# Performance work log

Hardware: AMD Instinct MI355X
Metric: run time of the kernel (lower is better)

## Reference

```python
import jax, jax.numpy as jnp
import numpy as np
import math

D_MODEL, HEADS, KQ = 1024, 16, 64
B, S = 2, 2048

def setup_inputs() -> dict:
    key = jax.random.key(0)
    k1, k2, k3, k4, k5 = jax.random.split(key, 5)
    scale = D_MODEL ** (-0.5)
    return {
        "x_BSE": jax.random.normal(k1, (B, S, D_MODEL), dtype=jnp.float32),
        "w_q": jax.random.normal(k2, (D_MODEL, HEADS, KQ), dtype=jnp.float32) * scale,
        "w_k": jax.random.normal(k3, (D_MODEL, HEADS, KQ), dtype=jnp.float32) * scale,
        "w_v": jax.random.normal(k4, (D_MODEL, HEADS, KQ), dtype=jnp.float32) * scale,
        "w_o": jax.random.normal(k5, (D_MODEL, HEADS, KQ), dtype=jnp.float32) * scale,
    }

def reference(x_BSE, w_q, w_k, w_v, w_o):
    # QKV projections (self-attention: memory = x)
    q_BSHK = jnp.einsum('BSE,EHK->BSHK', x_BSE, w_q)
    k_BMHK = jnp.einsum('BSE,EHK->BSHK', x_BSE, w_k)
    v_BMHK = jnp.einsum('BSE,EHK->BSHK', x_BSE, w_v)
    logits_BSHM = jnp.einsum('BSHK,BMHK->BSHM', q_BSHK, k_BMHK) / math.sqrt(KQ)
    # causal (diagonal) mask: query position >= memory position
    Sdim, Mdim = logits_BSHM.shape[1], logits_BSHM.shape[3]
    qpos = jnp.arange(Sdim)[:, None]          # [S,1]
    mpos = jnp.arange(Mdim)[None, :]          # [1,M]
    mask_SM = jnp.where(qpos >= mpos, 0.0, -jnp.inf).astype(logits_BSHM.dtype)
    logits_BSHM = logits_BSHM + mask_SM[None, :, None, :]
    probs_BSHM = jax.nn.softmax(logits_BSHM, axis=3)
    out_BSHK = jnp.einsum('BSHM,BMHK->BSHK', probs_BSHM, v_BMHK)
    return jnp.einsum('BSHK,EHK->BSE', out_BSHK, w_o)
```

## Files before the change

### kernel.cpp

```cpp
#include <hip/hip_runtime.h>
#include <hip/hip_bf16.h>

typedef __attribute__((ext_vector_type(4)))  float f32x4;
typedef __attribute__((ext_vector_type(16))) float f32x16;
typedef __attribute__((ext_vector_type(8)))  short short8;
typedef __attribute__((ext_vector_type(4)))  short short4v;

__device__ __forceinline__ short f2bf(float f) {
  union { float f; unsigned u; } x; x.f = f;
  unsigned r = (x.u + 0x7FFFu + ((x.u >> 16) & 1u)) >> 16;
  return (short)r;
}
__device__ __forceinline__ unsigned cvtpk(float lo, float hi) {
  unsigned r;
  asm("v_cvt_pk_bf16_f32 %0, %1, %2" : "=v"(r) : "v"(lo), "v"(hi));
  return r;
}

__global__ __launch_bounds__(256) void k_cast(const float* __restrict__ in,
                                              short* __restrict__ out, int n4) {
  int i = blockIdx.x * 256 + threadIdx.x;
  if (i >= n4) return;
  f32x4 v = ((const f32x4*)in)[i];
  short4v s;
  s[0] = f2bf(v[0]); s[1] = f2bf(v[1]); s[2] = f2bf(v[2]); s[3] = f2bf(v[3]);
  ((short4v*)out)[i] = s;
}

__global__ __launch_bounds__(256) void k_pack(const float* __restrict__ wq,
                                              const float* __restrict__ wk,
                                              const float* __restrict__ wv,
                                              short* __restrict__ WT) {
  int nt = blockIdx.x, et = blockIdx.y, sel = blockIdx.z;
  const float* w = sel == 0 ? wq : (sel == 1 ? wk : wv);
  __shared__ float tile[64][65];
  int tid = threadIdx.x;
  int cl = tid & 63, rw = tid >> 6;
#pragma unroll
  for (int j = 0; j < 16; ++j) {
    int el = j * 4 + rw;
    tile[el][cl] = w[(size_t)(et * 64 + el) * 1024 + nt * 64 + cl];
  }
  __syncthreads();
#pragma unroll
  for (int j = 0; j < 16; ++j) {
    int nl = j * 4 + rw;
    int n = sel * 1024 + nt * 64 + nl;
    WT[(size_t)n * 1024 + et * 64 + cl] = f2bf(tile[cl][nl]);
  }
}

template <int EPI>
__global__ __launch_bounds__(256) void k_gemm(const short* __restrict__ A,
                                              const short* __restrict__ B,
                                              short* __restrict__ Qo, short* __restrict__ Ko,
                                              short* __restrict__ Vo, float* __restrict__ out,
                                              int M, int N, int K) {
  __shared__ short As[128][40];
  __shared__ short Bs[128][40];
  int tid = threadIdx.x;
  int bm = blockIdx.y * 128, bn = blockIdx.x * 128;
  int wid = tid >> 6, lane = tid & 63;
  int wm = (wid >> 1) * 64, wn = (wid & 1) * 64;
  int lg = lane >> 4, lr = lane & 15;
  f32x4 acc[4][4] = {};

  int sr = tid >> 2, sc = tid & 3;
  const short* Ar0 = A + (size_t)(bm + sr) * K;
  const short* Ar1 = A + (size_t)(bm + sr + 64) * K;
  const short* Br0 = B + (size_t)(bn + sr) * K;
  const short* Br1 = B + (size_t)(bn + sr + 64) * K;

  short8 pa0 = *(const short8*)&Ar0[sc * 8];
  short8 pa1 = *(const short8*)&Ar1[sc * 8];
  short8 pb0 = *(const short8*)&Br0[sc * 8];
  short8 pb1 = *(const short8*)&Br1[sc * 8];

  int nk = K >> 5;
  for (int kt = 0; kt < nk; ++kt) {
    __syncthreads();
    *(short8*)&As[sr][sc * 8] = pa0;
    *(short8*)&As[sr + 64][sc * 8] = pa1;
    *(short8*)&Bs[sr][sc * 8] = pb0;
    *(short8*)&Bs[sr + 64][sc * 8] = pb1;
    if (kt + 1 < nk) {
      int ko = (kt + 1) * 32;
      pa0 = *(const short8*)&Ar0[ko + sc * 8];
      pa1 = *(const short8*)&Ar1[ko + sc * 8];
      pb0 = *(const short8*)&Br0[ko + sc * 8];
      pb1 = *(const short8*)&Br1[ko + sc * 8];
    }
    __syncthreads();
    short8 af[4], bf_[4];
#pragma unroll
    for (int mt = 0; mt < 4; ++mt)
      af[mt] = *(const short8*)&As[wm + mt * 16 + lr][lg * 8];
#pragma unroll
    for (int ntl = 0; ntl < 4; ++ntl)
      bf_[ntl] = *(const short8*)&Bs[wn + ntl * 16 + lr][lg * 8];
#pragma unroll
    for (int mt = 0; mt < 4; ++mt)
#pragma unroll
      for (int ntl = 0; ntl < 4; ++ntl)
        acc[mt][ntl] = __builtin_amdgcn_mfma_f32_16x16x32_bf16(af[mt], bf_[ntl], acc[mt][ntl], 0, 0, 0);
  }

#pragma unroll
  for (int mt = 0; mt < 4; ++mt)
#pragma unroll
    for (int ntl = 0; ntl < 4; ++ntl)
#pragma unroll
      for (int rr = 0; rr < 4; ++rr) {
        int m = bm + wm + mt * 16 + lg * 4 + rr;
        int n = bn + wn + ntl * 16 + lr;
        float val = acc[mt][ntl][rr];
        if (EPI == 0) {
          int b = m >> 11, s = m & 2047;
          int sel = n >> 10, hk = n & 1023;
          int h = hk >> 6, kd = hk & 63;
          if (sel == 0) Qo[((size_t)(b * 16 + h) * 2048 + s) * 64 + kd] = f2bf(val * 0.18033688011112042f);
          else if (sel == 1) Ko[((size_t)(b * 16 + h) * 2048 + s) * 64 + kd] = f2bf(val);
          else Vo[((size_t)(b * 16 + h) * 64 + kd) * 2048 + s] = f2bf(val);
        } else {
          out[(size_t)m * 1024 + n] = val;
        }
      }
}

__global__ __launch_bounds__(128, 2) void k_attn(const short* __restrict__ Q,
                                                 const short* __restrict__ K,
                                                 const short* __restrict__ VT,
                                                 short* __restrict__ O) {
  const int S = 2048;
  int bh = blockIdx.x;
  int g = 31 - blockIdx.y;

  int tid = threadIdx.x;
  int wid = tid >> 6, lane = tid & 63;
  int hi = lane >> 5, ln = lane & 31;
  int qw = 2 * g + wid;
  int ntile = qw + 1;
  int tmax = 2 * g + 2;
  int q_g = qw * 32 + ln;

  __shared__ short Ks[2][32][64];
  __shared__ short Vs[2][64][32];

  const short* Qb = Q + (size_t)bh * S * 64;
  const short* Kb = K + (size_t)bh * S * 64;
  const short* Vb = VT + (size_t)bh * 64 * S;

  short8 qf[4];
#pragma unroll
  for (int ds = 0; ds < 4; ++ds)
    qf[ds] = *(const short8*)&Qb[(size_t)q_g * 64 + ds * 16 + hi * 8];

  int kr = tid >> 2, kcb = tid & 3;
  int vd = tid >> 1, vcb = tid & 1;
  const short* kgp = Kb + (size_t)kr * 64;
  const short* vgp = Vb + (size_t)vd * S;

  short8 kreg0 = *(const short8*)&kgp[(size_t)0 + kcb * 8];
  short8 kreg1 = *(const short8*)&kgp[(size_t)0 + (kcb + 4) * 8];
  short8 vreg0 = *(const short8*)&vgp[(size_t)0 + vcb * 8];
  short8 vreg1 = *(const short8*)&vgp[(size_t)0 + (vcb + 2) * 8];

  f32x16 acoA = {}, acoB = {};
  float l = 0.f;

  for (int t = 0; t < tmax; ++t) {
    int buf = t & 1;
    *(short8*)&Ks[buf][kr][(kcb ^ (kr & 7)) * 8]       = kreg0;
    *(short8*)&Ks[buf][kr][((kcb + 4) ^ (kr & 7)) * 8] = kreg1;
    *(short8*)&Vs[buf][vd][(vcb ^ (vd & 3)) * 8]       = vreg0;
    *(short8*)&Vs[buf][vd][((vcb + 2) ^ (vd & 3)) * 8] = vreg1;
    if (t + 1 < tmax) {
      size_t ko = (size_t)(t + 1) * 32 * 64;
      size_t vo = (size_t)(t + 1) * 32;
      kreg0 = *(const short8*)&kgp[ko + kcb * 8];
      kreg1 = *(const short8*)&kgp[ko + (kcb + 4) * 8];
      vreg0 = *(const short8*)&vgp[vo + vcb * 8];
      vreg1 = *(const short8*)&vgp[vo + (vcb + 2) * 8];
    }
    __syncthreads();

    if (t < ntile) {
      short8 kc0 = *(const short8*)&Ks[buf][ln][((0 + hi) ^ (ln & 7)) * 8];
      short8 kc1 = *(const short8*)&Ks[buf][ln][((2 + hi) ^ (ln & 7)) * 8];
      short8 kc2 = *(const short8*)&Ks[buf][ln][((4 + hi) ^ (ln & 7)) * 8];
      short8 kc3 = *(const short8*)&Ks[buf][ln][((6 + hi) ^ (ln & 7)) * 8];
      f32x16 sa = {};
      __builtin_amdgcn_s_setprio(1);
      sa = __builtin_amdgcn_mfma_f32_32x32x16_bf16(kc0, qf[0], sa, 0, 0, 0);
      sa = __builtin_amdgcn_mfma_f32_32x32x16_bf16(kc1, qf[1], sa, 0, 0, 0);
      sa = __builtin_amdgcn_mfma_f32_32x32x16_bf16(kc2, qf[2], sa, 0, 0, 0);
      sa = __builtin_amdgcn_mfma_f32_32x32x16_bf16(kc3, qf[3], sa, 0, 0, 0);
      __builtin_amdgcn_s_setprio(0);

      if (t == qw) {
#pragma unroll
        for (int r = 0; r < 16; ++r) {
          int kv_g = t * 32 + (r & 3) + 8 * (r >> 2) + 4 * hi;
          if (kv_g > q_g) sa[r] = -1e30f;
        }
      }

      short8 v00 = *(const short8*)&Vs[buf][ln][((0 + hi) ^ (ln & 3)) * 8];
      short8 v01 = *(const short8*)&Vs[buf][ln][((2 + hi) ^ (ln & 3)) * 8];
      short8 v10 = *(const short8*)&Vs[buf][32 + ln][((0 + hi) ^ (ln & 3)) * 8];
      short8 v11 = *(const short8*)&Vs[buf][32 + ln][((2 + hi) ^ (ln & 3)) * 8];

      float p[16];
#pragma unroll
      for (int r = 0; r < 16; ++r) p[r] = exp2f(sa[r]);
      float s0 = (p[0] + p[1]) + (p[2] + p[3]);
      float s1 = (p[4] + p[5]) + (p[6] + p[7]);
      float s2 = (p[8] + p[9]) + (p[10] + p[11]);
      float s3 = (p[12] + p[13]) + (p[14] + p[15]);
      l += (s0 + s1) + (s2 + s3);

#pragma unroll
      for (int s = 0; s < 2; ++s) {
        unsigned c0 = cvtpk(p[8 * s + 0], p[8 * s + 1]);
        unsigned c1 = cvtpk(p[8 * s + 2], p[8 * s + 3]);
        unsigned c2 = cvtpk(p[8 * s + 4], p[8 * s + 5]);
        unsigned c3 = cvtpk(p[8 * s + 6], p[8 * s + 7]);
        unsigned pc0 = (unsigned)__shfl_xor((int)c0, 32);
        unsigned pc1 = (unsigned)__shfl_xor((int)c1, 32);
        unsigned pc2 = (unsigned)__shfl_xor((int)c2, 32);
        unsigned pc3 = (unsigned)__shfl_xor((int)c3, 32);
        union { unsigned u[4]; short8 v; } pb;
        pb.u[0] = hi ? pc2 : c0;
        pb.u[1] = hi ? pc3 : c1;
        pb.u[2] = hi ? c2 : pc0;
        pb.u[3] = hi ? c3 : pc1;
        __builtin_amdgcn_s_setprio(1);
        if (s == 0) {
          acoA = __builtin_amdgcn_mfma_f32_32x32x16_bf16(v00, pb.v, acoA, 0, 0, 0);
          acoB = __builtin_amdgcn_mfma_f32_32x32x16_bf16(v10, pb.v, acoB, 0, 0, 0);
        } else {
          acoA = __builtin_amdgcn_mfma_f32_32x32x16_bf16(v01, pb.v, acoA, 0, 0, 0);
          acoB = __builtin_amdgcn_mfma_f32_32x32x16_bf16(v11, pb.v, acoB, 0, 0, 0);
        }
        __builtin_amdgcn_s_setprio(0);
      }
    }
  }

  l += __shfl_xor(l, 32);
  float rl = 1.f / l;
  int b = bh >> 4, h = bh & 15;
  size_t obase = ((size_t)b * 2048 + q_g) * 1024 + h * 64;
#pragma unroll
  for (int g4 = 0; g4 < 4; ++g4) {
    int d0 = 8 * g4 + 4 * hi;
    *(unsigned*)&O[obase + d0]          = cvtpk(acoA[4 * g4] * rl, acoA[4 * g4 + 1] * rl);
    *(unsigned*)&O[obase + d0 + 2]      = cvtpk(acoA[4 * g4 + 2] * rl, acoA[4 * g4 + 3] * rl);
    *(unsigned*)&O[obase + 32 + d0]     = cvtpk(acoB[4 * g4] * rl, acoB[4 * g4 + 1] * rl);
    *(unsigned*)&O[obase + 32 + d0 + 2] = cvtpk(acoB[4 * g4 + 2] * rl, acoB[4 * g4 + 3] * rl);
  }
}

extern "C" void kernel_launch(void* const* d_in, const int* in_sizes, int n_in,
                              void* d_out, int out_size, void* d_ws, size_t ws_size,
                              hipStream_t stream) {
  const float* x  = (const float*)d_in[0];
  const float* wq = (const float*)d_in[1];
  const float* wk = (const float*)d_in[2];
  const float* wv = (const float*)d_in[3];
  const float* wo = (const float*)d_in[4];
  float* out = (float*)d_out;
  char* ws = (char*)d_ws;

  short* x_bf  = (short*)(ws);
  short* WqkvT = (short*)(ws + ((size_t)8 << 20));
  short* wo_bf = (short*)(ws + ((size_t)14 << 20));
  short* Qb    = (short*)(ws + ((size_t)16 << 20));
  short* Kb    = (short*)(ws + ((size_t)24 << 20));
  short* Vt    = (short*)(ws + ((size_t)32 << 20));
  short* Ob    = (short*)(ws + ((size_t)40 << 20));

  k_cast<<<4096, 256, 0, stream>>>(x, x_bf, 1048576);
  k_cast<<<1024, 256, 0, stream>>>(wo, wo_bf, 262144);
  k_pack<<<dim3(16, 16, 3), 256, 0, stream>>>(wq, wk, wv, WqkvT);
  k_gemm<0><<<dim3(24, 32), 256, 0, stream>>>(x_bf, WqkvT, Qb, Kb, Vt, nullptr, 4096, 3072, 1024);
  k_attn<<<dim3(32, 32), 128, 0, stream>>>(Qb, Kb, Vt, Ob);
  k_gemm<1><<<dim3(8, 32), 256, 0, stream>>>(Ob, wo_bf, nullptr, nullptr, nullptr, out, 4096, 1024, 1024);
}
```

Measured before the change: 130.9 us.

## Split causal attention KV range in two halves and merge partials

```diff
diff --git a/kernel.cpp b/kernel.cpp
--- a/kernel.cpp
+++ b/kernel.cpp
@@ -10,6 +10,10 @@
   union { float f; unsigned u; } x; x.f = f;
   unsigned r = (x.u + 0x7FFFu + ((x.u >> 16) & 1u)) >> 16;
   return (short)r;
+}
+__device__ __forceinline__ float bf2f(short s) {
+  union { unsigned u; float f; } x; x.u = ((unsigned)(unsigned short)s) << 16;
+  return x.f;
 }
 __device__ __forceinline__ unsigned cvtpk(float lo, float hi) {
   unsigned r;
@@ -127,21 +131,26 @@
       }
 }
 
-__global__ __launch_bounds__(128, 2) void k_attn(const short* __restrict__ Q,
+__global__ __launch_bounds__(128, 4) void k_attn(const short* __restrict__ Q,
                                                  const short* __restrict__ K,
                                                  const short* __restrict__ VT,
-                                                 short* __restrict__ O) {
+                                                 short* __restrict__ P0,
+                                                 short* __restrict__ P1,
+                                                 float* __restrict__ ML) {
   const int S = 2048;
   int bh = blockIdx.x;
-  int g = 31 - blockIdx.y;
+  int y = blockIdx.y;
+  int h = y & 1;
+  int g = 31 - (y >> 1);
 
   int tid = threadIdx.x;
   int wid = tid >> 6, lane = tid & 63;
   int hi = lane >> 5, ln = lane & 31;
   int qw = 2 * g + wid;
-  int ntile = qw + 1;
-  int tmax = 2 * g + 2;
   int q_g = qw * 32 + ln;
+  int tb = h * (g + 1);
+  int nstage = g + 1;
+  int te_w = qw + 1;
 
   __shared__ short Ks[2][32][64];
   __shared__ short Vs[2][64][32];
@@ -160,22 +169,25 @@
   const short* kgp = Kb + (size_t)kr * 64;
   const short* vgp = Vb + (size_t)vd * S;
 
-  short8 kreg0 = *(const short8*)&kgp[(size_t)0 + kcb * 8];
-  short8 kreg1 = *(const short8*)&kgp[(size_t)0 + (kcb + 4) * 8];
-  short8 vreg0 = *(const short8*)&vgp[(size_t)0 + vcb * 8];
-  short8 vreg1 = *(const short8*)&vgp[(size_t)0 + (vcb + 2) * 8];
+  size_t ko0 = (size_t)tb * 2048;
+  size_t vo0 = (size_t)tb * 32;
+  short8 kreg0 = *(const short8*)&kgp[ko0 + kcb * 8];
+  short8 kreg1 = *(const short8*)&kgp[ko0 + (kcb + 4) * 8];
+  short8 vreg0 = *(const short8*)&vgp[vo0 + vcb * 8];
+  short8 vreg1 = *(const short8*)&vgp[vo0 + (vcb + 2) * 8];
 
   f32x16 acoA = {}, acoB = {};
   float l = 0.f;
 
-  for (int t = 0; t < tmax; ++t) {
-    int buf = t & 1;
+  for (int i = 0; i < nstage; ++i) {
+    int t = tb + i;
+    int buf = i & 1;
     *(short8*)&Ks[buf][kr][(kcb ^ (kr & 7)) * 8]       = kreg0;
     *(short8*)&Ks[buf][kr][((kcb + 4) ^ (kr & 7)) * 8] = kreg1;
     *(short8*)&Vs[buf][vd][(vcb ^ (vd & 3)) * 8]       = vreg0;
     *(short8*)&Vs[buf][vd][((vcb + 2) ^ (vd & 3)) * 8] = vreg1;
-    if (t + 1 < tmax) {
-      size_t ko = (size_t)(t + 1) * 32 * 64;
+    if (i + 1 < nstage) {
+      size_t ko = (size_t)(t + 1) * 2048;
       size_t vo = (size_t)(t + 1) * 32;
       kreg0 = *(const short8*)&kgp[ko + kcb * 8];
       kreg1 = *(const short8*)&kgp[ko + (kcb + 4) * 8];
@@ -184,7 +196,7 @@
     }
     __syncthreads();
 
-    if (t < ntile) {
+    if (t < te_w) {
       short8 kc0 = *(const short8*)&Ks[buf][ln][((0 + hi) ^ (ln & 7)) * 8];
       short8 kc1 = *(const short8*)&Ks[buf][ln][((2 + hi) ^ (ln & 7)) * 8];
       short8 kc2 = *(const short8*)&Ks[buf][ln][((4 + hi) ^ (ln & 7)) * 8];
@@ -248,17 +260,44 @@
   }
 
   l += __shfl_xor(l, 32);
-  float rl = 1.f / l;
-  int b = bh >> 4, h = bh & 15;
-  size_t obase = ((size_t)b * 2048 + q_g) * 1024 + h * 64;
+  int row = (bh << 11) + q_g;
+  ML[row * 2 + h] = l;
+  short* Op = h ? P1 : P0;
+  size_t base = (size_t)row * 64;
 #pragma unroll
   for (int g4 = 0; g4 < 4; ++g4) {
     int d0 = 8 * g4 + 4 * hi;
-    *(unsigned*)&O[obase + d0]          = cvtpk(acoA[4 * g4] * rl, acoA[4 * g4 + 1] * rl);
-    *(unsigned*)&O[obase + d0 + 2]      = cvtpk(acoA[4 * g4 + 2] * rl, acoA[4 * g4 + 3] * rl);
-    *(unsigned*)&O[obase + 32 + d0]     = cvtpk(acoB[4 * g4] * rl, acoB[4 * g4 + 1] * rl);
-    *(unsigned*)&O[obase + 32 + d0 + 2] = cvtpk(acoB[4 * g4 + 2] * rl, acoB[4 * g4 + 3] * rl);
-  }
+    *(unsigned*)&Op[base + d0]          = cvtpk(acoA[4 * g4], acoA[4 * g4 + 1]);
+    *(unsigned*)&Op[base + d0 + 2]      = cvtpk(acoA[4 * g4 + 2], acoA[4 * g4 + 3]);
+    *(unsigned*)&Op[base + 32 + d0]     = cvtpk(acoB[4 * g4], acoB[4 * g4 + 1]);
+    *(unsigned*)&Op[base + 32 + d0 + 2] = cvtpk(acoB[4 * g4 + 2], acoB[4 * g4 + 3]);
+  }
+}
+
+__global__ __launch_bounds__(256) void k_merge(const short* __restrict__ P0,
+                                               const short* __restrict__ P1,
+                                               const float* __restrict__ ML,
+                                               short* __restrict__ O) {
+  int gi = blockIdx.x * 256 + threadIdx.x;
+  int row = gi >> 2;
+  int dc = (gi & 3) << 4;
+  float w = 1.f / (ML[row * 2] + ML[row * 2 + 1]);
+  size_t pbase = (size_t)row * 64 + dc;
+  short8 a0 = *(const short8*)&P0[pbase];
+  short8 a1 = *(const short8*)&P0[pbase + 8];
+  short8 b0 = *(const short8*)&P1[pbase];
+  short8 b1 = *(const short8*)&P1[pbase + 8];
+  int bh = row >> 11, q = row & 2047;
+  int b = bh >> 4, h = bh & 15;
+  size_t obase = ((size_t)b * 2048 + q) * 1024 + h * 64 + dc;
+  short8 o0, o1;
+#pragma unroll
+  for (int j = 0; j < 8; ++j) {
+    o0[j] = f2bf((bf2f(a0[j]) + bf2f(b0[j])) * w);
+    o1[j] = f2bf((bf2f(a1[j]) + bf2f(b1[j])) * w);
+  }
+  *(short8*)&O[obase] = o0;
+  *(short8*)&O[obase + 8] = o1;
 }
 
 extern "C" void kernel_launch(void* const* d_in, const int* in_sizes, int n_in,
@@ -279,11 +318,15 @@
   short* Kb    = (short*)(ws + ((size_t)24 << 20));
   short* Vt    = (short*)(ws + ((size_t)32 << 20));
   short* Ob    = (short*)(ws + ((size_t)40 << 20));
+  short* P0    = (short*)(ws);
+  float* ML    = (float*)(ws + ((size_t)8 << 20));
+  short* P1    = (short*)(ws + ((size_t)48 << 20));
 
   k_cast<<<4096, 256, 0, stream>>>(x, x_bf, 1048576);
   k_cast<<<1024, 256, 0, stream>>>(wo, wo_bf, 262144);
   k_pack<<<dim3(16, 16, 3), 256, 0, stream>>>(wq, wk, wv, WqkvT);
   k_gemm<0><<<dim3(24, 32), 256, 0, stream>>>(x_bf, WqkvT, Qb, Kb, Vt, nullptr, 4096, 3072, 1024);
-  k_attn<<<dim3(32, 32), 128, 0, stream>>>(Qb, Kb, Vt, Ob);
+  k_attn<<<dim3(32, 64), 128, 0, stream>>>(Qb, Kb, Vt, P0, P1, ML);
+  k_merge<<<1024, 256, 0, stream>>>(P0, P1, ML, Ob);
   k_gemm<1><<<dim3(8, 32), 256, 0, stream>>>(Ob, wo_bf, nullptr, nullptr, nullptr, out, 4096, 1024, 1024);
 }
```

Result: slower. 138.5 us (+5.8%).

## Process KV tiles in pairs per barrier with interleaved QK MFMA chains

Applied to the files above, without the earlier changes.

```diff
diff --git a/kernel.cpp b/kernel.cpp
--- a/kernel.cpp
+++ b/kernel.cpp
@@ -139,12 +139,11 @@
   int wid = tid >> 6, lane = tid & 63;
   int hi = lane >> 5, ln = lane & 31;
   int qw = 2 * g + wid;
-  int ntile = qw + 1;
-  int tmax = 2 * g + 2;
   int q_g = qw * 32 + ln;
-
-  __shared__ short Ks[2][32][64];
-  __shared__ short Vs[2][64][32];
+  int npair = g + 1;
+
+  __shared__ short Ks[2][2][32][64];
+  __shared__ short Vs[2][2][64][32];
 
   const short* Qb = Q + (size_t)bh * S * 64;
   const short* Kb = K + (size_t)bh * S * 64;
@@ -160,87 +159,155 @@
   const short* kgp = Kb + (size_t)kr * 64;
   const short* vgp = Vb + (size_t)vd * S;
 
-  short8 kreg0 = *(const short8*)&kgp[(size_t)0 + kcb * 8];
-  short8 kreg1 = *(const short8*)&kgp[(size_t)0 + (kcb + 4) * 8];
-  short8 vreg0 = *(const short8*)&vgp[(size_t)0 + vcb * 8];
-  short8 vreg1 = *(const short8*)&vgp[(size_t)0 + (vcb + 2) * 8];
+  short8 ka0 = *(const short8*)&kgp[kcb * 8];
+  short8 ka1 = *(const short8*)&kgp[(kcb + 4) * 8];
+  short8 kb0 = *(const short8*)&kgp[2048 + kcb * 8];
+  short8 kb1 = *(const short8*)&kgp[2048 + (kcb + 4) * 8];
+  short8 va0 = *(const short8*)&vgp[vcb * 8];
+  short8 va1 = *(const short8*)&vgp[(vcb + 2) * 8];
+  short8 vb0 = *(const short8*)&vgp[32 + vcb * 8];
+  short8 vb1 = *(const short8*)&vgp[32 + (vcb + 2) * 8];
 
   f32x16 acoA = {}, acoB = {};
   float l = 0.f;
 
-  for (int t = 0; t < tmax; ++t) {
-    int buf = t & 1;
-    *(short8*)&Ks[buf][kr][(kcb ^ (kr & 7)) * 8]       = kreg0;
-    *(short8*)&Ks[buf][kr][((kcb + 4) ^ (kr & 7)) * 8] = kreg1;
-    *(short8*)&Vs[buf][vd][(vcb ^ (vd & 3)) * 8]       = vreg0;
-    *(short8*)&Vs[buf][vd][((vcb + 2) ^ (vd & 3)) * 8] = vreg1;
-    if (t + 1 < tmax) {
-      size_t ko = (size_t)(t + 1) * 32 * 64;
-      size_t vo = (size_t)(t + 1) * 32;
-      kreg0 = *(const short8*)&kgp[ko + kcb * 8];
-      kreg1 = *(const short8*)&kgp[ko + (kcb + 4) * 8];
-      vreg0 = *(const short8*)&vgp[vo + vcb * 8];
-      vreg1 = *(const short8*)&vgp[vo + (vcb + 2) * 8];
+  for (int p = 0; p < npair; ++p) {
+    int pb = p & 1;
+    *(short8*)&Ks[pb][0][kr][(kcb ^ (kr & 7)) * 8]       = ka0;
+    *(short8*)&Ks[pb][0][kr][((kcb + 4) ^ (kr & 7)) * 8] = ka1;
+    *(short8*)&Ks[pb][1][kr][(kcb ^ (kr & 7)) * 8]       = kb0;
+    *(short8*)&Ks[pb][1][kr][((kcb + 4) ^ (kr & 7)) * 8] = kb1;
+    *(short8*)&Vs[pb][0][vd][(vcb ^ (vd & 3)) * 8]       = va0;
+    *(short8*)&Vs[pb][0][vd][((vcb + 2) ^ (vd & 3)) * 8] = va1;
+    *(short8*)&Vs[pb][1][vd][(vcb ^ (vd & 3)) * 8]       = vb0;
+    *(short8*)&Vs[pb][1][vd][((vcb + 2) ^ (vd & 3)) * 8] = vb1;
+    if (p + 1 < npair) {
+      size_t ko0 = (size_t)(2 * p + 2) * 2048, ko1 = (size_t)(2 * p + 3) * 2048;
+      size_t vo0 = (size_t)(2 * p + 2) * 32,   vo1 = (size_t)(2 * p + 3) * 32;
+      ka0 = *(const short8*)&kgp[ko0 + kcb * 8];
+      ka1 = *(const short8*)&kgp[ko0 + (kcb + 4) * 8];
+      kb0 = *(const short8*)&kgp[ko1 + kcb * 8];
+      kb1 = *(const short8*)&kgp[ko1 + (kcb + 4) * 8];
+      va0 = *(const short8*)&vgp[vo0 + vcb * 8];
+      va1 = *(const short8*)&vgp[vo0 + (vcb + 2) * 8];
+      vb0 = *(const short8*)&vgp[vo1 + vcb * 8];
+      vb1 = *(const short8*)&vgp[vo1 + (vcb + 2) * 8];
     }
     __syncthreads();
 
-    if (t < ntile) {
-      short8 kc0 = *(const short8*)&Ks[buf][ln][((0 + hi) ^ (ln & 7)) * 8];
-      short8 kc1 = *(const short8*)&Ks[buf][ln][((2 + hi) ^ (ln & 7)) * 8];
-      short8 kc2 = *(const short8*)&Ks[buf][ln][((4 + hi) ^ (ln & 7)) * 8];
-      short8 kc3 = *(const short8*)&Ks[buf][ln][((6 + hi) ^ (ln & 7)) * 8];
-      f32x16 sa = {};
-      __builtin_amdgcn_s_setprio(1);
-      sa = __builtin_amdgcn_mfma_f32_32x32x16_bf16(kc0, qf[0], sa, 0, 0, 0);
-      sa = __builtin_amdgcn_mfma_f32_32x32x16_bf16(kc1, qf[1], sa, 0, 0, 0);
-      sa = __builtin_amdgcn_mfma_f32_32x32x16_bf16(kc2, qf[2], sa, 0, 0, 0);
-      sa = __builtin_amdgcn_mfma_f32_32x32x16_bf16(kc3, qf[3], sa, 0, 0, 0);
-      __builtin_amdgcn_s_setprio(0);
-
-      if (t == qw) {
-#pragma unroll
-        for (int r = 0; r < 16; ++r) {
-          int kv_g = t * 32 + (r & 3) + 8 * (r >> 2) + 4 * hi;
-          if (kv_g > q_g) sa[r] = -1e30f;
-        }
-      }
-
-      short8 v00 = *(const short8*)&Vs[buf][ln][((0 + hi) ^ (ln & 3)) * 8];
-      short8 v01 = *(const short8*)&Vs[buf][ln][((2 + hi) ^ (ln & 3)) * 8];
-      short8 v10 = *(const short8*)&Vs[buf][32 + ln][((0 + hi) ^ (ln & 3)) * 8];
-      short8 v11 = *(const short8*)&Vs[buf][32 + ln][((2 + hi) ^ (ln & 3)) * 8];
-
-      float p[16];
-#pragma unroll
-      for (int r = 0; r < 16; ++r) p[r] = exp2f(sa[r]);
-      float s0 = (p[0] + p[1]) + (p[2] + p[3]);
-      float s1 = (p[4] + p[5]) + (p[6] + p[7]);
-      float s2 = (p[8] + p[9]) + (p[10] + p[11]);
-      float s3 = (p[12] + p[13]) + (p[14] + p[15]);
-      l += (s0 + s1) + (s2 + s3);
-
+    int t0 = 2 * p, t1 = 2 * p + 1;
+
+    short8 kc00 = *(const short8*)&Ks[pb][0][ln][((0 + hi) ^ (ln & 7)) * 8];
+    short8 kc01 = *(const short8*)&Ks[pb][0][ln][((2 + hi) ^ (ln & 7)) * 8];
+    short8 kc02 = *(const short8*)&Ks[pb][0][ln][((4 + hi) ^ (ln & 7)) * 8];
+    short8 kc03 = *(const short8*)&Ks[pb][0][ln][((6 + hi) ^ (ln & 7)) * 8];
+    short8 kc10 = *(const short8*)&Ks[pb][1][ln][((0 + hi) ^ (ln & 7)) * 8];
+    short8 kc11 = *(const short8*)&Ks[pb][1][ln][((2 + hi) ^ (ln & 7)) * 8];
+    short8 kc12 = *(const short8*)&Ks[pb][1][ln][((4 + hi) ^ (ln & 7)) * 8];
+    short8 kc13 = *(const short8*)&Ks[pb][1][ln][((6 + hi) ^ (ln & 7)) * 8];
+
+    f32x16 sa0 = {}, sa1 = {};
+    __builtin_amdgcn_s_setprio(1);
+    sa0 = __builtin_amdgcn_mfma_f32_32x32x16_bf16(kc00, qf[0], sa0, 0, 0, 0);
+    sa1 = __builtin_amdgcn_mfma_f32_32x32x16_bf16(kc10, qf[0], sa1, 0, 0, 0);
+    sa0 = __builtin_amdgcn_mfma_f32_32x32x16_bf16(kc01, qf[1], sa0, 0, 0, 0);
+    sa1 = __builtin_amdgcn_mfma_f32_32x32x16_bf16(kc11, qf[1], sa1, 0, 0, 0);
+    sa0 = __builtin_amdgcn_mfma_f32_32x32x16_bf16(kc02, qf[2], sa0, 0, 0, 0);
+    sa1 = __builtin_amdgcn_mfma_f32_32x32x16_bf16(kc12, qf[2], sa1, 0, 0, 0);
+    sa0 = __builtin_amdgcn_mfma_f32_32x32x16_bf16(kc03, qf[3], sa0, 0, 0, 0);
+    sa1 = __builtin_amdgcn_mfma_f32_32x32x16_bf16(kc13, qf[3], sa1, 0, 0, 0);
+    __builtin_amdgcn_s_setprio(0);
+
+    if (t0 >= qw) {
+#pragma unroll
+      for (int r = 0; r < 16; ++r) {
+        int kv_g = t0 * 32 + (r & 3) + 8 * (r >> 2) + 4 * hi;
+        if (kv_g > q_g) sa0[r] = -1e30f;
+      }
+    }
+    if (t1 >= qw) {
+#pragma unroll
+      for (int r = 0; r < 16; ++r) {
+        int kv_g = t1 * 32 + (r & 3) + 8 * (r >> 2) + 4 * hi;
+        if (kv_g > q_g) sa1[r] = -1e30f;
+      }
+    }
+
+    float p0[16], p1[16];
+#pragma unroll
+    for (int r = 0; r < 16; ++r) p0[r] = exp2f(sa0[r]);
+#pragma unroll
+    for (int r = 0; r < 16; ++r) p1[r] = exp2f(sa1[r]);
+    {
+      float s00 = (p0[0] + p0[1]) + (p0[2] + p0[3]);
+      float s01 = (p0[4] + p0[5]) + (p0[6] + p0[7]);
+      float s02 = (p0[8] + p0[9]) + (p0[10] + p0[11]);
+      float s03 = (p0[12] + p0[13]) + (p0[14] + p0[15]);
+      float s10 = (p1[0] + p1[1]) + (p1[2] + p1[3]);
+      float s11 = (p1[4] + p1[5]) + (p1[6] + p1[7]);
+      float s12 = (p1[8] + p1[9]) + (p1[10] + p1[11]);
+      float s13 = (p1[12] + p1[13]) + (p1[14] + p1[15]);
+      l += ((s00 + s01) + (s02 + s03)) + ((s10 + s11) + (s12 + s13));
+    }
+
+    {
+      short8 v00 = *(const short8*)&Vs[pb][0][ln][((0 + hi) ^ (ln & 3)) * 8];
+      short8 v01 = *(const short8*)&Vs[pb][0][ln][((2 + hi) ^ (ln & 3)) * 8];
+      short8 v10 = *(const short8*)&Vs[pb][0][32 + ln][((0 + hi) ^ (ln & 3)) * 8];
+      short8 v11 = *(const short8*)&Vs[pb][0][32 + ln][((2 + hi) ^ (ln & 3)) * 8];
 #pragma unroll
       for (int s = 0; s < 2; ++s) {
-        unsigned c0 = cvtpk(p[8 * s + 0], p[8 * s + 1]);
-        unsigned c1 = cvtpk(p[8 * s + 2], p[8 * s + 3]);
-        unsigned c2 = cvtpk(p[8 * s + 4], p[8 * s + 5]);
-        unsigned c3 = cvtpk(p[8 * s + 6], p[8 * s + 7]);
+        unsigned c0 = cvtpk(p0[8 * s + 0], p0[8 * s + 1]);
+        unsigned c1 = cvtpk(p0[8 * s + 2], p0[8 * s + 3]);
+        unsigned c2 = cvtpk(p0[8 * s + 4], p0[8 * s + 5]);
+        unsigned c3 = cvtpk(p0[8 * s + 6], p0[8 * s + 7]);
         unsigned pc0 = (unsigned)__shfl_xor((int)c0, 32);
         unsigned pc1 = (unsigned)__shfl_xor((int)c1, 32);
         unsigned pc2 = (unsigned)__shfl_xor((int)c2, 32);
         unsigned pc3 = (unsigned)__shfl_xor((int)c3, 32);
-        union { unsigned u[4]; short8 v; } pb;
-        pb.u[0] = hi ? pc2 : c0;
-        pb.u[1] = hi ? pc3 : c1;
-        pb.u[2] = hi ? c2 : pc0;
-        pb.u[3] = hi ? c3 : pc1;
+        union { unsigned u[4]; short8 v; } pbv;
+        pbv.u[0] = hi ? pc2 : c0;
+        pbv.u[1] = hi ? pc3 : c1;
+        pbv.u[2] = hi ? c2 : pc0;
+        pbv.u[3] = hi ? c3 : pc1;
         __builtin_amdgcn_s_setprio(1);
         if (s == 0) {
-          acoA = __builtin_amdgcn_mfma_f32_32x32x16_bf16(v00, pb.v, acoA, 0, 0, 0);
-          acoB = __builtin_amdgcn_mfma_f32_32x32x16_bf16(v10, pb.v, acoB, 0, 0, 0);
+          acoA = __builtin_amdgcn_mfma_f32_32x32x16_bf16(v00, pbv.v, acoA, 0, 0, 0);
+          acoB = __builtin_amdgcn_mfma_f32_32x32x16_bf16(v10, pbv.v, acoB, 0, 0, 0);
         } else {
-          acoA = __builtin_amdgcn_mfma_f32_32x32x16_bf16(v01, pb.v, acoA, 0, 0, 0);
-          acoB = __builtin_amdgcn_mfma_f32_32x32x16_bf16(v11, pb.v, acoB, 0, 0, 0);
+          acoA = __builtin_amdgcn_mfma_f32_32x32x16_bf16(v01, pbv.v, acoA, 0, 0, 0);
+          acoB = __builtin_amdgcn_mfma_f32_32x32x16_bf16(v11, pbv.v, acoB, 0, 0, 0);
+        }
+        __builtin_amdgcn_s_setprio(0);
+      }
+    }
+    {
+      short8 v00 = *(const short8*)&Vs[pb][1][ln][((0 + hi) ^ (ln & 3)) * 8];
+      short8 v01 = *(const short8*)&Vs[pb][1][ln][((2 + hi) ^ (ln & 3)) * 8];
+      short8 v10 = *(const short8*)&Vs[pb][1][32 + ln][((0 + hi) ^ (ln & 3)) * 8];
+      short8 v11 = *(const short8*)&Vs[pb][1][32 + ln][((2 + hi) ^ (ln & 3)) * 8];
+#pragma unroll
+      for (int s = 0; s < 2; ++s) {
+        unsigned c0 = cvtpk(p1[8 * s + 0], p1[8 * s + 1]);
+        unsigned c1 = cvtpk(p1[8 * s + 2], p1[8 * s + 3]);
+        unsigned c2 = cvtpk(p1[8 * s + 4], p1[8 * s + 5]);
+        unsigned c3 = cvtpk(p1[8 * s + 6], p1[8 * s + 7]);
+        unsigned pc0 = (unsigned)__shfl_xor((int)c0, 32);
+        unsigned pc1 = (unsigned)__shfl_xor((int)c1, 32);
+        unsigned pc2 = (unsigned)__shfl_xor((int)c2, 32);
+        unsigned pc3 = (unsigned)__shfl_xor((int)c3, 32);
+        union { unsigned u[4]; short8 v; } pbv;
+        pbv.u[0] = hi ? pc2 : c0;
+        pbv.u[1] = hi ? pc3 : c1;
+        pbv.u[2] = hi ? c2 : pc0;
+        pbv.u[3] = hi ? c3 : pc1;
+        __builtin_amdgcn_s_setprio(1);
+        if (s == 0) {
+          acoA = __builtin_amdgcn_mfma_f32_32x32x16_bf16(v00, pbv.v, acoA, 0, 0, 0);
+          acoB = __builtin_amdgcn_mfma_f32_32x32x16_bf16(v10, pbv.v, acoB, 0, 0, 0);
+        } else {
+          acoA = __builtin_amdgcn_mfma_f32_32x32x16_bf16(v01, pbv.v, acoA, 0, 0, 0);
+          acoB = __builtin_amdgcn_mfma_f32_32x32x16_bf16(v11, pbv.v, acoB, 0, 0, 0);
         }
         __builtin_amdgcn_s_setprio(0);
       }
```

Measured after the change: 129.7 us. Within noise of the previous version (-0.9%).

## Process KV tiles in pairs with two-deep register prefetch in attention

Applied to the files above, without the earlier changes.

```diff
diff --git a/kernel.cpp b/kernel.cpp
--- a/kernel.cpp
+++ b/kernel.cpp
@@ -108,23 +108,34 @@
 #pragma unroll
   for (int mt = 0; mt < 4; ++mt)
 #pragma unroll
-    for (int ntl = 0; ntl < 4; ++ntl)
-#pragma unroll
-      for (int rr = 0; rr < 4; ++rr) {
-        int m = bm + wm + mt * 16 + lg * 4 + rr;
-        int n = bn + wn + ntl * 16 + lr;
-        float val = acc[mt][ntl][rr];
-        if (EPI == 0) {
-          int b = m >> 11, s = m & 2047;
-          int sel = n >> 10, hk = n & 1023;
-          int h = hk >> 6, kd = hk & 63;
-          if (sel == 0) Qo[((size_t)(b * 16 + h) * 2048 + s) * 64 + kd] = f2bf(val * 0.18033688011112042f);
-          else if (sel == 1) Ko[((size_t)(b * 16 + h) * 2048 + s) * 64 + kd] = f2bf(val);
-          else Vo[((size_t)(b * 16 + h) * 64 + kd) * 2048 + s] = f2bf(val);
+    for (int ntl = 0; ntl < 4; ++ntl) {
+      int m0 = bm + wm + mt * 16 + lg * 4;
+      int n = bn + wn + ntl * 16 + lr;
+      if (EPI == 0) {
+        int b = m0 >> 11, s0 = m0 & 2047;
+        int sel = n >> 10, hk = n & 1023;
+        int h = hk >> 6, kd = hk & 63;
+        if (sel == 0) {
+#pragma unroll
+          for (int rr = 0; rr < 4; ++rr)
+            Qo[((size_t)(b * 16 + h) * 2048 + s0 + rr) * 64 + kd] =
+                f2bf(acc[mt][ntl][rr] * 0.18033688011112042f);
+        } else if (sel == 1) {
+#pragma unroll
+          for (int rr = 0; rr < 4; ++rr)
+            Ko[((size_t)(b * 16 + h) * 2048 + s0 + rr) * 64 + kd] = f2bf(acc[mt][ntl][rr]);
         } else {
-          out[(size_t)m * 1024 + n] = val;
+          short4v v4;
+#pragma unroll
+          for (int rr = 0; rr < 4; ++rr) v4[rr] = f2bf(acc[mt][ntl][rr]);
+          *(short4v*)&Vo[((size_t)(b * 16 + h) * 64 + kd) * 2048 + s0] = v4;
         }
+      } else {
+#pragma unroll
+        for (int rr = 0; rr < 4; ++rr)
+          out[(size_t)(m0 + rr) * 1024 + n] = acc[mt][ntl][rr];
       }
+    }
 }
 
 __global__ __launch_bounds__(128, 2) void k_attn(const short* __restrict__ Q,
@@ -139,12 +150,11 @@
   int wid = tid >> 6, lane = tid & 63;
   int hi = lane >> 5, ln = lane & 31;
   int qw = 2 * g + wid;
-  int ntile = qw + 1;
-  int tmax = 2 * g + 2;
   int q_g = qw * 32 + ln;
-
-  __shared__ short Ks[2][32][64];
-  __shared__ short Vs[2][64][32];
+  int npair = g + 1;
+
+  __shared__ short Ks[2][2][32][64];
+  __shared__ short Vs[2][2][64][32];
 
   const short* Qb = Q + (size_t)bh * S * 64;
   const short* Kb = K + (size_t)bh * S * 64;
@@ -160,92 +170,172 @@
   const short* kgp = Kb + (size_t)kr * 64;
   const short* vgp = Vb + (size_t)vd * S;
 
-  short8 kreg0 = *(const short8*)&kgp[(size_t)0 + kcb * 8];
-  short8 kreg1 = *(const short8*)&kgp[(size_t)0 + (kcb + 4) * 8];
-  short8 vreg0 = *(const short8*)&vgp[(size_t)0 + vcb * 8];
-  short8 vreg1 = *(const short8*)&vgp[(size_t)0 + (vcb + 2) * 8];
+  short8 Aka0, Aka1, Akb0, Akb1, Ava0, Ava1, Avb0, Avb1;
+  short8 Bka0, Bka1, Bkb0, Bkb1, Bva0, Bva1, Bvb0, Bvb1;
+
+#define LOADP(SET, pn)                                                        \
+  {                                                                           \
+    size_t ko0 = (size_t)(2 * (pn)) * 2048, ko1 = (size_t)(2 * (pn) + 1) * 2048; \
+    size_t vo0 = (size_t)(2 * (pn)) * 32,   vo1 = (size_t)(2 * (pn) + 1) * 32;   \
+    SET##ka0 = *(const short8*)&kgp[ko0 + kcb * 8];                           \
+    SET##ka1 = *(const short8*)&kgp[ko0 + (kcb + 4) * 8];                     \
+    SET##kb0 = *(const short8*)&kgp[ko1 + kcb * 8];                           \
+    SET##kb1 = *(const short8*)&kgp[ko1 + (kcb + 4) * 8];                     \
+    SET##va0 = *(const short8*)&vgp[vo0 + vcb * 8];                           \
+    SET##va1 = *(const short8*)&vgp[vo0 + (vcb + 2) * 8];                     \
+    SET##vb0 = *(const short8*)&vgp[vo1 + vcb * 8];                           \
+    SET##vb1 = *(const short8*)&vgp[vo1 + (vcb + 2) * 8];                     \
+  }
+
+#define WRITEP(SET, BUF)                                                      \
+  {                                                                           \
+    *(short8*)&Ks[BUF][0][kr][(kcb ^ (kr & 7)) * 8]       = SET##ka0;         \
+    *(short8*)&Ks[BUF][0][kr][((kcb + 4) ^ (kr & 7)) * 8] = SET##ka1;         \
+    *(short8*)&Ks[BUF][1][kr][(kcb ^ (kr & 7)) * 8]       = SET##kb0;         \
+    *(short8*)&Ks[BUF][1][kr][((kcb + 4) ^ (kr & 7)) * 8] = SET##kb1;         \
+    *(short8*)&Vs[BUF][0][vd][(vcb ^ (vd & 3)) * 8]       = SET##va0;         \
+    *(short8*)&Vs[BUF][0][vd][((vcb + 2) ^ (vd & 3)) * 8] = SET##va1;         \
+    *(short8*)&Vs[BUF][1][vd][(vcb ^ (vd & 3)) * 8]       = SET##vb0;         \
+    *(short8*)&Vs[BUF][1][vd][((vcb + 2) ^ (vd & 3)) * 8] = SET##vb1;         \
+  }
 
   f32x16 acoA = {}, acoB = {};
   float l = 0.f;
 
-  for (int t = 0; t < tmax; ++t) {
-    int buf = t & 1;
-    *(short8*)&Ks[buf][kr][(kcb ^ (kr & 7)) * 8]       = kreg0;
-    *(short8*)&Ks[buf][kr][((kcb + 4) ^ (kr & 7)) * 8] = kreg1;
-    *(short8*)&Vs[buf][vd][(vcb ^ (vd & 3)) * 8]       = vreg0;
-    *(short8*)&Vs[buf][vd][((vcb + 2) ^ (vd & 3)) * 8] = vreg1;
-    if (t + 1 < tmax) {
-      size_t ko = (size_t)(t + 1) * 32 * 64;
-      size_t vo = (size_t)(t + 1) * 32;
-      kreg0 = *(const short8*)&kgp[ko + kcb * 8];
-      kreg1 = *(const short8*)&kgp[ko + (kcb + 4) * 8];
-      vreg0 = *(const short8*)&vgp[vo + vcb * 8];
-      vreg1 = *(const short8*)&vgp[vo + (vcb + 2) * 8];
+#define COMPUTE_PAIR(BUF, P)                                                  \
+  {                                                                           \
+    int t0 = 2 * (P), t1 = 2 * (P) + 1;                                       \
+    short8 kc00 = *(const short8*)&Ks[BUF][0][ln][((0 + hi) ^ (ln & 7)) * 8]; \
+    short8 kc01 = *(const short8*)&Ks[BUF][0][ln][((2 + hi) ^ (ln & 7)) * 8]; \
+    short8 kc02 = *(const short8*)&Ks[BUF][0][ln][((4 + hi) ^ (ln & 7)) * 8]; \
+    short8 kc03 = *(const short8*)&Ks[BUF][0][ln][((6 + hi) ^ (ln & 7)) * 8]; \
+    short8 kc10 = *(const short8*)&Ks[BUF][1][ln][((0 + hi) ^ (ln & 7)) * 8]; \
+    short8 kc11 = *(const short8*)&Ks[BUF][1][ln][((2 + hi) ^ (ln & 7)) * 8]; \
+    short8 kc12 = *(const short8*)&Ks[BUF][1][ln][((4 + hi) ^ (ln & 7)) * 8]; \
+    short8 kc13 = *(const short8*)&Ks[BUF][1][ln][((6 + hi) ^ (ln & 7)) * 8]; \
+    f32x16 sa0 = {}, sa1 = {};                                                \
+    __builtin_amdgcn_s_setprio(1);                                            \
+    sa0 = __builtin_amdgcn_mfma_f32_32x32x16_bf16(kc00, qf[0], sa0, 0, 0, 0); \
+    sa1 = __builtin_amdgcn_mfma_f32_32x32x16_bf16(kc10, qf[0], sa1, 0, 0, 0); \
+    sa0 = __builtin_amdgcn_mfma_f32_32x32x16_bf16(kc01, qf[1], sa0, 0, 0, 0); \
+    sa1 = __builtin_amdgcn_mfma_f32_32x32x16_bf16(kc11, qf[1], sa1, 0, 0, 0); \
+    sa0 = __builtin_amdgcn_mfma_f32_32x32x16_bf16(kc02, qf[2], sa0, 0, 0, 0); \
+    sa1 = __builtin_amdgcn_mfma_f32_32x32x16_bf16(kc12, qf[2], sa1, 0, 0, 0); \
+    sa0 = __builtin_amdgcn_mfma_f32_32x32x16_bf16(kc03, qf[3], sa0, 0, 0, 0); \
+    sa1 = __builtin_amdgcn_mfma_f32_32x32x16_bf16(kc13, qf[3], sa1, 0, 0, 0); \
+    __builtin_amdgcn_s_setprio(0);                                            \
+    if (t0 >= qw) {                                                           \
+      _Pragma("unroll")                                                       \
+      for (int r = 0; r < 16; ++r) {                                          \
+        int kv_g = t0 * 32 + (r & 3) + 8 * (r >> 2) + 4 * hi;                 \
+        if (kv_g > q_g) sa0[r] = -1e30f;                                      \
+      }                                                                       \
+    }                                                                         \
+    if (t1 >= qw) {                                                           \
+      _Pragma("unroll")                                                       \
+      for (int r = 0; r < 16; ++r) {                                          \
+        int kv_g = t1 * 32 + (r & 3) + 8 * (r >> 2) + 4 * hi;                 \
+        if (kv_g > q_g) sa1[r] = -1e30f;                                      \
+      }                                                                       \
+    }                                                                         \
+    float p0[16], p1[16];                                                     \
+    _Pragma("unroll")                                                         \
+    for (int r = 0; r < 16; ++r) p0[r] = exp2f(sa0[r]);                       \
+    _Pragma("unroll")                                                         \
+    for (int r = 0; r < 16; ++r) p1[r] = exp2f(sa1[r]);                       \
+    {                                                                         \
+      float s00 = (p0[0] + p0[1]) + (p0[2] + p0[3]);                          \
+      float s01 = (p0[4] + p0[5]) + (p0[6] + p0[7]);                          \
+      float s02 = (p0[8] + p0[9]) + (p0[10] + p0[11]);                        \
+      float s03 = (p0[12] + p0[13]) + (p0[14] + p0[15]);                      \
+      float s10 = (p1[0] + p1[1]) + (p1[2] + p1[3]);                          \
+      float s11 = (p1[4] + p1[5]) + (p1[6] + p1[7]);                          \
+      float s12 = (p1[8] + p1[9]) + (p1[10] + p1[11]);                        \
+      float s13 = (p1[12] + p1[13]) + (p1[14] + p1[15]);                      \
+      l += ((s00 + s01) + (s02 + s03)) + ((s10 + s11) + (s12 + s13));         \
+    }                                                                         \
+    {                                                                         \
+      short8 v00 = *(const short8*)&Vs[BUF][0][ln][((0 + hi) ^ (ln & 3)) * 8];\
+      short8 v01 = *(const short8*)&Vs[BUF][0][ln][((2 + hi) ^ (ln & 3)) * 8];\
+      short8 v10 = *(const short8*)&Vs[BUF][0][32 + ln][((0 + hi) ^ (ln & 3)) * 8];\
+      short8 v11 = *(const short8*)&Vs[BUF][0][32 + ln][((2 + hi) ^ (ln & 3)) * 8];\
+      _Pragma("unroll")                                                       \
+      for (int s = 0; s < 2; ++s) {                                           \
+        unsigned c0 = cvtpk(p0[8 * s + 0], p0[8 * s + 1]);                    \
+        unsigned c1 = cvtpk(p0[8 * s + 2], p0[8 * s + 3]);                    \
+        unsigned c2 = cvtpk(p0[8 * s + 4], p0[8 * s + 5]);                    \
+        unsigned c3 = cvtpk(p0[8 * s + 6], p0[8 * s + 7]);                    \
+        unsigned pc0 = (unsigned)__shfl_xor((int)c0, 32);                     \
+        unsigned pc1 = (unsigned)__shfl_xor((int)c1, 32);                     \
+        unsigned pc2 = (unsigned)__shfl_xor((int)c2, 32);                     \
+        unsigned pc3 = (unsigned)__shfl_xor((int)c3, 32);                     \
+        union { unsigned u[4]; short8 v; } pbv;                               \
+        pbv.u[0] = hi ? pc2 : c0;                                             \
+        pbv.u[1] = hi ? pc3 : c1;                                             \
+        pbv.u[2] = hi ? c2 : pc0;                                             \
+        pbv.u[3] = hi ? c3 : pc1;                                             \
+        __builtin_amdgcn_s_setprio(1);                                        \
+        if (s == 0) {                                                         \
+          acoA = __builtin_amdgcn_mfma_f32_32x32x16_bf16(v00, pbv.v, acoA, 0, 0, 0);\
+          acoB = __builtin_amdgcn_mfma_f32_32x32x16_bf16(v10, pbv.v, acoB, 0, 0, 0);\
+        } else {                                                              \
+          acoA = __builtin_amdgcn_mfma_f32_32x32x16_bf16(v01, pbv.v, acoA, 0, 0, 0);\
+          acoB = __builtin_amdgcn_mfma_f32_32x32x16_bf16(v11, pbv.v, acoB, 0, 0, 0);\
+        }                                                                     \
+        __builtin_amdgcn_s_setprio(0);                                        \
+      }                                                                       \
+    }                                                                         \
+    {                                                                         \
+      short8 v00 = *(const short8*)&Vs[BUF][1][ln][((0 + hi) ^ (ln & 3)) * 8];\
+      short8 v01 = *(const short8*)&Vs[BUF][1][ln][((2 + hi) ^ (ln & 3)) * 8];\
+      short8 v10 = *(const short8*)&Vs[BUF][1][32 + ln][((0 + hi) ^ (ln & 3)) * 8];\
+      short8 v11 = *(const short8*)&Vs[BUF][1][32 + ln][((2 + hi) ^ (ln & 3)) * 8];\
+      _Pragma("unroll")                                                       \
+      for (int s = 0; s < 2; ++s) {                                           \
+        unsigned c0 = cvtpk(p1[8 * s + 0], p1[8 * s + 1]);                    \
+        unsigned c1 = cvtpk(p1[8 * s + 2], p1[8 * s + 3]);                    \
+        unsigned c2 = cvtpk(p1[8 * s + 4], p1[8 * s + 5]);                    \
+        unsigned c3 = cvtpk(p1[8 * s + 6], p1[8 * s + 7]);                    \
+        unsigned pc0 = (unsigned)__shfl_xor((int)c0, 32);                     \
+        unsigned pc1 = (unsigned)__shfl_xor((int)c1, 32);                     \
+        unsigned pc2 = (unsigned)__shfl_xor((int)c2, 32);                     \
+        unsigned pc3 = (unsigned)__shfl_xor((int)c3, 32);                     \
+        union { unsigned u[4]; short8 v; } pbv;                               \
+        pbv.u[0] = hi ? pc2 : c0;                                             \
+        pbv.u[1] = hi ? pc3 : c1;                                             \
+        pbv.u[2] = hi ? c2 : pc0;                                             \
+        pbv.u[3] = hi ? c3 : pc1;                                             \
+        __builtin_amdgcn_s_setprio(1);                                        \
+        if (s == 0) {                                                         \
+          acoA = __builtin_amdgcn_mfma_f32_32x32x16_bf16(v00, pbv.v, acoA, 0, 0, 0);\
+          acoB = __builtin_amdgcn_mfma_f32_32x32x16_bf16(v10, pbv.v, acoB, 0, 0, 0);\
+        } else {                                                              \
+          acoA = __builtin_amdgcn_mfma_f32_32x32x16_bf16(v01, pbv.v, acoA, 0, 0, 0);\
+          acoB = __builtin_amdgcn_mfma_f32_32x32x16_bf16(v11, pbv.v, acoB, 0, 0, 0);\
+        }                                                                     \
+        __builtin_amdgcn_s_setprio(0);                                        \
+      }                                                                       \
+    }                                                                         \
+  }
+
+  LOADP(A, 0)
+  if (npair > 1) LOADP(B, 1)
+
+  for (int pp = 0; pp < npair; pp += 2) {
+    WRITEP(A, 0)
+    if (pp + 2 < npair) LOADP(A, pp + 2)
+    __syncthreads();
+    COMPUTE_PAIR(0, pp)
+    if (pp + 1 < npair) {
+      WRITEP(B, 1)
+      if (pp + 3 < npair) LOADP(B, pp + 3)
+      __syncthreads();
+      COMPUTE_PAIR(1, pp + 1)
     }
-    __syncthreads();
-
-    if (t < ntile) {
-      short8 kc0 = *(const short8*)&Ks[buf][ln][((0 + hi) ^ (ln & 7)) * 8];
-      short8 kc1 = *(const short8*)&Ks[buf][ln][((2 + hi) ^ (ln & 7)) * 8];
-      short8 kc2 = *(const short8*)&Ks[buf][ln][((4 + hi) ^ (ln & 7)) * 8];
-      short8 kc3 = *(const short8*)&Ks[buf][ln][((6 + hi) ^ (ln & 7)) * 8];
-      f32x16 sa = {};
-      __builtin_amdgcn_s_setprio(1);
-      sa = __builtin_amdgcn_mfma_f32_32x32x16_bf16(kc0, qf[0], sa, 0, 0, 0);
-      sa = __builtin_amdgcn_mfma_f32_32x32x16_bf16(kc1, qf[1], sa, 0, 0, 0);
-      sa = __builtin_amdgcn_mfma_f32_32x32x16_bf16(kc2, qf[2], sa, 0, 0, 0);
-      sa = __builtin_amdgcn_mfma_f32_32x32x16_bf16(kc3, qf[3], sa, 0, 0, 0);
-      __builtin_amdgcn_s_setprio(0);
-
-      if (t == qw) {
-#pragma unroll
-        for (int r = 0; r < 16; ++r) {
-          int kv_g = t * 32 + (r & 3) + 8 * (r >> 2) + 4 * hi;
-          if (kv_g > q_g) sa[r] = -1e30f;
-        }
-      }
-
-      short8 v00 = *(const short8*)&Vs[buf][ln][((0 + hi) ^ (ln & 3)) * 8];
-      short8 v01 = *(const short8*)&Vs[buf][ln][((2 + hi) ^ (ln & 3)) * 8];
-      short8 v10 = *(const short8*)&Vs[buf][32 + ln][((0 + hi) ^ (ln & 3)) * 8];
-      short8 v11 = *(const short8*)&Vs[buf][32 + ln][((2 + hi) ^ (ln & 3)) * 8];
-
-      float p[16];
-#pragma unroll
-      for (int r = 0; r < 16; ++r) p[r] = exp2f(sa[r]);
-      float s0 = (p[0] + p[1]) + (p[2] + p[3]);
-      float s1 = (p[4] + p[5]) + (p[6] + p[7]);
-      float s2 = (p[8] + p[9]) + (p[10] + p[11]);
-      float s3 = (p[12] + p[13]) + (p[14] + p[15]);
-      l += (s0 + s1) + (s2 + s3);
-
-#pragma unroll
-      for (int s = 0; s < 2; ++s) {
-        unsigned c0 = cvtpk(p[8 * s + 0], p[8 * s + 1]);
-        unsigned c1 = cvtpk(p[8 * s + 2], p[8 * s + 3]);
-        unsigned c2 = cvtpk(p[8 * s + 4], p[8 * s + 5]);
-        unsigned c3 = cvtpk(p[8 * s + 6], p[8 * s + 7]);
-        unsigned pc0 = (unsigned)__shfl_xor((int)c0, 32);
-        unsigned pc1 = (unsigned)__shfl_xor((int)c1, 32);
-        unsigned pc2 = (unsigned)__shfl_xor((int)c2, 32);
-        unsigned pc3 = (unsigned)__shfl_xor((int)c3, 32);
-        union { unsigned u[4]; short8 v; } pb;
-        pb.u[0] = hi ? pc2 : c0;
-        pb.u[1] = hi ? pc3 : c1;
-        pb.u[2] = hi ? c2 : pc0;
-        pb.u[3] = hi ? c3 : pc1;
-        __builtin_amdgcn_s_setprio(1);
-        if (s == 0) {
-          acoA = __builtin_amdgcn_mfma_f32_32x32x16_bf16(v00, pb.v, acoA, 0, 0, 0);
-          acoB = __builtin_amdgcn_mfma_f32_32x32x16_bf16(v10, pb.v, acoB, 0, 0, 0);
-        } else {
-          acoA = __builtin_amdgcn_mfma_f32_32x32x16_bf16(v01, pb.v, acoA, 0, 0, 0);
-          acoB = __builtin_amdgcn_mfma_f32_32x32x16_bf16(v11, pb.v, acoB, 0, 0, 0);
-        }
-        __builtin_amdgcn_s_setprio(0);
-      }
-    }
-  }
+  }
+#undef LOADP
+#undef WRITEP
+#undef COMPUTE_PAIR
 
   l += __shfl_xor(l, 32);
   float rl = 1.f / l;
```

Result: faster. 123.4 us (-5.7%).
